# Kernel tuning notes

Hardware: AMD Instinct MI355X
Metric: run time of the kernel (lower is better)

The kernel has to match this reference:

```python
import jax, jax.numpy as jnp
import numpy as np

T, D, R, C, L = 4096, 512, 32, 32, 2  # time, input, trace, context, num_blocks
NEG_SLOPE = 0.01
EPS = 1e-5  # eqx LayerNorm default


def _layernorm(x, g, b):
    m = jnp.mean(x, -1, keepdims=True)
    v = jnp.var(x, -1, keepdims=True)
    return g * (x - m) * jax.lax.rsqrt(v + EPS) + b


def _ffa_scan(a, b, pre, s0, start):
    # a:[R], b:[C], pre:[T,R,C] real>=0, s0:[1,R,C] complex64, start:[T] bool
    ab = jax.lax.complex(jnp.broadcast_to(-jnp.abs(a)[:, None], (R, C)),
                         jnp.broadcast_to(b[None, :], (R, C)))  # log decay+rotation
    ts = jnp.concatenate([jnp.zeros((1,), jnp.float32), jnp.ones((T,), jnp.float32)])
    vals = jnp.concatenate([s0, pre.astype(jnp.complex64)], axis=0)  # [T+1,R,C]
    rst = jnp.concatenate([jnp.zeros((1,), bool), start])

    def op(l, r):
        tl, sl, dl = l
        tr, sr, dr = r
        decay = jnp.exp(ab[None, :, :] * tr[:, None, None])  # gamma^{t_r}
        s = jnp.where(dr[:, None, None], sr, sr + sl * decay)
        t = jnp.where(dr, tr, tl + tr)
        return (t, s, dl | dr)

    _, states, _ = jax.lax.associative_scan(op, (ts, vals, rst))
    return states[1:]  # [T,R,C]


def _forward(x, start_b, state_real, state_imag, Wt, Wc, a, b,
             W0, b0, g0, beta0, W1, b1, g1, beta1):
    h = x
    z = x
    for i in range(L):
        tr = h @ Wt[i].T  # [T,R]
        ct = h @ Wc[i].T  # [T,R] (source maps context proj to trace_size too; R==C)
        pre = jnp.abs(tr[:, :, None] * ct[:, None, :])  # [T,R,C] outer product
        pre = pre / (1e-8 + jnp.sum(pre, axis=(-2, -1), keepdims=True))
        s0 = jax.lax.complex(state_real[i], state_imag[i])  # [1,R,C]
        states = _ffa_scan(a[i], b[i], pre, s0, start_b)
        s = states.reshape(T, R * C)
        mag = jnp.log1p(jnp.abs(s))
        ang = jnp.angle(s)
        scaled = jnp.concatenate([mag * jnp.sin(ang), mag * jnp.cos(ang)], axis=-1)  # [T,2RC]
        z = jax.nn.leaky_relu(_layernorm(scaled @ W0[i].T + b0[i], g0[i], beta0[i]), NEG_SLOPE)
        z = jax.nn.leaky_relu(_layernorm(z @ W1[i].T + b1[i], g1[i], beta1[i]), NEG_SLOPE)
        h = h + z  # residual feeds next block; NSFFM returns last block's z
    return z


def setup_inputs() -> dict:
    key = jax.random.key(0)
    ks = jax.random.split(key, 8)
    x = jax.random.normal(ks[0], (T, D), jnp.float32)
    start = jax.random.randint(ks[1], (T,), 0, 2).astype(jnp.int32)
    next_done = jax.random.randint(ks[2], (T,), 0, 2).astype(jnp.int32)
    Wt = jax.random.normal(ks[3], (L, R, D), jnp.float32) / np.sqrt(D)
    Wc = jax.random.normal(ks[4], (L, R, D), jnp.float32) / np.sqrt(D)
    # ffa.init: a = linspace decays, b = log-spaced angular frequencies
    a = jnp.broadcast_to(jnp.linspace(1e-6, 0.5, R, dtype=jnp.float32)[None], (L, R)).copy()
    b = jnp.broadcast_to((2 * jnp.pi / jnp.exp(jnp.linspace(np.log(1.0), np.log(1024.0), C))).astype(jnp.float32)[None], (L, C)).copy()
    W0 = jax.random.normal(ks[5], (L, D, 2 * R * C), jnp.float32) * 0.01  # default_init scale=0.01
    W1 = jax.random.normal(ks[6], (L, D, D), jnp.float32) / np.sqrt(D)
    return {
        'x': x, 'start': start, 'next_done': next_done,
        'state_real': jnp.zeros((L, 1, R, C), jnp.float32),
        'state_imag': jnp.zeros((L, 1, R, C), jnp.float32),
        'Wt': Wt, 'Wc': Wc, 'a': a, 'b': b,
        'W0': W0, 'b0': jnp.zeros((L, D), jnp.float32),
        'g0': jnp.ones((L, D), jnp.float32), 'beta0': jnp.zeros((L, D), jnp.float32),
        'W1': W1, 'b1': jnp.zeros((L, D), jnp.float32),
        'g1': jnp.ones((L, D), jnp.float32), 'beta1': jnp.zeros((L, D), jnp.float32),
    }


def reference(x, start, next_done, state_real, state_imag, Wt, Wc, a, b,
              W0, b0, g0, beta0, W1, b1, g1, beta1):
    del next_done  # not used in the scan math (kept for interface parity)
    start_b = start.astype(bool)
    return _forward(x, start_b, state_real, state_imag, Wt, Wc, a, b,
                    W0, b0, g0, beta0, W1, b1, g1, beta1)
```

## Files before the change

kernel.cpp:

```cpp
#include <hip/hip_runtime.h>
#include <math.h>

#define TT 4096
#define DD 512
#define RR 32
#define CC 32
#define RC 1024
#define LL 2
#define CHUNK 32
#define NCHUNK 128
#define NEG_SLOPE 0.01f
#define LN_EPS 1e-5f

typedef __attribute__((ext_vector_type(8))) __bf16 bf16x8;
typedef __attribute__((ext_vector_type(4))) float f32x4;

__device__ __forceinline__ unsigned short f2bf(float f) {
    unsigned int u = __builtin_bit_cast(unsigned int, f);
    u += 0x7fffu + ((u >> 16) & 1u);
    return (unsigned short)(u >> 16);
}

#define NX4  524288
#define NW04 524288
#define NW14 131072
#define NCV  (NX4 + NW04 + NW14)
#define NPK  16384
__global__ __launch_bounds__(256) void setup_kernel(const float4* __restrict__ x,
                                                    const float4* __restrict__ W0,
                                                    const float4* __restrict__ W1,
                                                    const float* __restrict__ Wt,
                                                    const float* __restrict__ Wc,
                                                    ushort4* __restrict__ xb,
                                                    ushort4* __restrict__ W0b,
                                                    ushort4* __restrict__ W1b,
                                                    ushort4* __restrict__ Wtc) {
    int i = blockIdx.x * 256 + threadIdx.x;
    float4 v;
    ushort4* dst;
    int j;
    if (i < NCV) {
        const float4* src;
        if (i < NX4) { src = x; dst = xb; j = i; }
        else if (i < NX4 + NW04) { src = W0; dst = W0b; j = i - NX4; }
        else { src = W1; dst = W1b; j = i - NX4 - NW04; }
        v = src[j];
    } else {
        int ii = i - NCV;
        if (ii >= NPK) return;
        int e = ii * 4;
        int l = e >> 15;
        int r = (e >> 9) & 63;
        int k = e & 511;
        v = (r < 32) ? *(const float4*)&Wt[((size_t)l * 32 + r) * 512 + k]
                     : *(const float4*)&Wc[((size_t)l * 32 + (r - 32)) * 512 + k];
        dst = Wtc; j = ii;
    }
    ushort4 o;
    o.x = f2bf(v.x); o.y = f2bf(v.y); o.z = f2bf(v.z); o.w = f2bf(v.w);
    dst[j] = o;
}

__global__ __launch_bounds__(256) void proj_denom_kernel(const unsigned short* __restrict__ A,
                                                         const unsigned short* __restrict__ B,
                                                         float* __restrict__ tcabs) {
    __shared__ __align__(16) unsigned short As[64 * 32];
    __shared__ __align__(16) unsigned short Bs[64 * 32];
    const int tid = threadIdx.x;
    const int w = tid >> 6, lane = tid & 63;
    const int bm = blockIdx.x * 64;
    const int K = 512;
    const int srow = tid >> 2;
    const int sl = tid & 3;
    const int sswz = (sl ^ ((srow >> 1) & 3)) * 8;
    const unsigned short* gA = A + (size_t)(bm + srow) * K + sl * 8;
    const unsigned short* gB = B + (size_t)srow * K + sl * 8;
    const int wA = srow * 32 + sswz;
    const int wB = srow * 32 + sswz;
    const int fr = lane & 15, hi = lane >> 4;
    const int kslot = hi ^ ((fr >> 1) & 3);
    f32x4 acc0 = {}, acc1 = {}, acc2 = {}, acc3 = {};

    uint4 va = *(const uint4*)gA;
    uint4 vb = *(const uint4*)gB;
    for (int k0 = 0; k0 < K; k0 += 32) {
        __syncthreads();
        *(uint4*)&As[wA] = va;
        *(uint4*)&Bs[wB] = vb;
        __syncthreads();
        if (k0 + 32 < K) {
            va = *(const uint4*)(gA + k0 + 32);
            vb = *(const uint4*)(gB + k0 + 32);
        }
        const int arow = w * 16 + fr;
        bf16x8 af = *(const bf16x8*)&As[arow * 32 + kslot * 8];
        bf16x8 b0 = *(const bf16x8*)&Bs[(0 * 16 + fr) * 32 + kslot * 8];
        bf16x8 b1 = *(const bf16x8*)&Bs[(1 * 16 + fr) * 32 + kslot * 8];
        bf16x8 b2 = *(const bf16x8*)&Bs[(2 * 16 + fr) * 32 + kslot * 8];
        bf16x8 b3 = *(const bf16x8*)&Bs[(3 * 16 + fr) * 32 + kslot * 8];
        acc0 = __builtin_amdgcn_mfma_f32_16x16x32_bf16(af, b0, acc0, 0, 0, 0);
        acc1 = __builtin_amdgcn_mfma_f32_16x16x32_bf16(af, b1, acc1, 0, 0, 0);
        acc2 = __builtin_amdgcn_mfma_f32_16x16x32_bf16(af, b2, acc2, 0, 0, 0);
        acc3 = __builtin_amdgcn_mfma_f32_16x16x32_bf16(af, b3, acc3, 0, 0, 0);
    }
#pragma unroll
    for (int q = 0; q < 4; ++q) {
        float a0 = fabsf(acc0[q]), a1 = fabsf(acc1[q]);
        float a2 = fabsf(acc2[q]), a3 = fabsf(acc3[q]);
        float st = a0 + a1, sc = a2 + a3;
        st += __shfl_xor(st, 1); sc += __shfl_xor(sc, 1);
        st += __shfl_xor(st, 2); sc += __shfl_xor(sc, 2);
        st += __shfl_xor(st, 4); sc += __shfl_xor(sc, 4);
        st += __shfl_xor(st, 8); sc += __shfl_xor(sc, 8);
        float inv = 1.f / (1e-8f + st * sc);
        size_t rb = (size_t)(bm + w * 16 + hi * 4 + q) * 64;
        tcabs[rb + fr]      = a0 * inv;
        tcabs[rb + fr + 16] = a1 * inv;
        tcabs[rb + fr + 32] = a2;
        tcabs[rb + fr + 48] = a3;
    }
}

__global__ __launch_bounds__(256) void scan_pass1(const float* __restrict__ tcabs,
                                                  const int* __restrict__ start,
                                                  const float* __restrict__ a,
                                                  const float* __restrict__ b,
                                                  float4* __restrict__ ab4) {
    int tid = blockIdx.x * 256 + threadIdx.x;
    int rc = tid & (RC - 1);
    int chunk = tid >> 10;
    int r = rc >> 5, c = rc & 31;
    float e = expf(-fabsf(a[r]));
    float gr = e * cosf(b[c]);
    float gi = e * sinf(b[c]);
    float alr = 1.f, ali = 0.f, ber = 0.f, bei = 0.f;
    int t0 = chunk * CHUNK;
    for (int j = 0; j < CHUNK; ++j) {
        int t = t0 + j;
        float pre = tcabs[t * 64 + r] * tcabs[t * 64 + 32 + c];
        if (start[t]) {
            alr = 0.f; ali = 0.f; ber = pre; bei = 0.f;
        } else {
            float nbr = pre + gr * ber - gi * bei;
            float nbi =       gr * bei + gi * ber;
            float nar = gr * alr - gi * ali;
            float nai = gr * ali + gi * alr;
            ber = nbr; bei = nbi; alr = nar; ali = nai;
        }
    }
    ab4[chunk * RC + rc] = make_float4(alr, ali, ber, bei);
}

__global__ __launch_bounds__(256) void scan_pass2f(const float* __restrict__ tcabs,
                                                   const float4* __restrict__ ab4,
                                                   const int* __restrict__ start,
                                                   const float* __restrict__ a,
                                                   const float* __restrict__ b,
                                                   const float* __restrict__ s0r,
                                                   const float* __restrict__ s0i,
                                                   unsigned short* __restrict__ scaled) {
    int bx = blockIdx.x;
    int chunk = bx >> 2;
    int rc = (bx & 3) * 256 + threadIdx.x;
    int r = rc >> 5, c = rc & 31;
    float e = expf(-fabsf(a[r]));
    float gr = e * cosf(b[c]);
    float gi = e * sinf(b[c]);
    float sr = s0r[rc], si = s0i[rc];
    int j = 0;
    for (; j + 8 <= chunk; j += 8) {
        float4 buf[8];
#pragma unroll
        for (int u = 0; u < 8; ++u) buf[u] = ab4[(j + u) * RC + rc];
#pragma unroll
        for (int u = 0; u < 8; ++u) {
            float nsr = buf[u].z + buf[u].x * sr - buf[u].y * si;
            float nsi = buf[u].w + buf[u].x * si + buf[u].y * sr;
            sr = nsr; si = nsi;
        }
    }
    for (; j < chunk; ++j) {
        float4 ab = ab4[j * RC + rc];
        float nsr = ab.z + ab.x * sr - ab.y * si;
        float nsi = ab.w + ab.x * si + ab.y * sr;
        sr = nsr; si = nsi;
    }
    int t0 = chunk * CHUNK;
    for (int jj = 0; jj < CHUNK; ++jj) {
        int t = t0 + jj;
        float pre = tcabs[t * 64 + r] * tcabs[t * 64 + 32 + c];
        if (start[t]) {
            sr = pre; si = 0.f;
        } else {
            float nsr = pre + gr * sr - gi * si;
            float nsi =       gr * si + gi * sr;
            sr = nsr; si = nsi;
        }
        float m = sqrtf(sr * sr + si * si);
        float mag = log1pf(m);
        float f = (m > 0.f) ? (mag / m) : 0.f;
        scaled[(size_t)t * 2048 + rc]        = f2bf(si * f);
        scaled[(size_t)t * 2048 + 1024 + rc] = f2bf(sr * f);
    }
}

template <int K, int N, int SPLITK>
__global__ __launch_bounds__(256) void gemm_bt_mfma(const unsigned short* __restrict__ A,
                                                    const unsigned short* __restrict__ B,
                                                    float* __restrict__ Cm) {
    __shared__ __align__(16) unsigned short As[128 * 64];
    __shared__ __align__(16) unsigned short Bs[64 * 64];
    const int tid = threadIdx.x;
    const int w = tid >> 6, lane = tid & 63;
    const int nwg = gridDim.x * gridDim.y * gridDim.z;
    const int id = blockIdx.x + gridDim.x * (blockIdx.y + gridDim.y * blockIdx.z);
    const int lid = (id & 7) * (nwg >> 3) + (id >> 3);
    const int bxs = lid % gridDim.x;
    const int t2 = lid / gridDim.x;
    const int bys = t2 % gridDim.y;
    const int bzs = t2 / gridDim.y;
    const int bm = bys * 128, bn = bxs * 64;
    const int kbeg = bzs * (K / SPLITK);
    const int kend = kbeg + (K / SPLITK);
    const int wr = w >> 1, wc = w & 1;
    const int srow = tid >> 3;
    const int k8 = tid & 7;
    const int swz = (k8 ^ (srow & 7)) * 8;
    const unsigned short* gA = A + (size_t)(bm + srow) * K + k8 * 8;
    const unsigned short* gB = B + (size_t)(bn + srow) * K + k8 * 8;
    const int wAb = srow * 64 + swz;
    const int fr = lane & 15, hi = lane >> 4;
    f32x4 acc[4][2] = {};

    uint4 va0 = *(const uint4*)(gA + kbeg);
    uint4 va1 = *(const uint4*)(gA + (size_t)32 * K + kbeg);
    uint4 va2 = *(const uint4*)(gA + (size_t)64 * K + kbeg);
    uint4 va3 = *(const uint4*)(gA + (size_t)96 * K + kbeg);
    uint4 vb0 = *(const uint4*)(gB + kbeg);
    uint4 vb1 = *(const uint4*)(gB + (size_t)32 * K + kbeg);
    for (int k0 = kbeg; k0 < kend; k0 += 64) {
        __syncthreads();
        *(uint4*)&As[wAb]        = va0;
        *(uint4*)&As[wAb + 2048] = va1;
        *(uint4*)&As[wAb + 4096] = va2;
        *(uint4*)&As[wAb + 6144] = va3;
        *(uint4*)&Bs[wAb]        = vb0;
        *(uint4*)&Bs[wAb + 2048] = vb1;
        __syncthreads();
        if (k0 + 64 < kend) {
            va0 = *(const uint4*)(gA + k0 + 64);
            va1 = *(const uint4*)(gA + (size_t)32 * K + k0 + 64);
            va2 = *(const uint4*)(gA + (size_t)64 * K + k0 + 64);
            va3 = *(const uint4*)(gA + (size_t)96 * K + k0 + 64);
            vb0 = *(const uint4*)(gB + k0 + 64);
            vb1 = *(const uint4*)(gB + (size_t)32 * K + k0 + 64);
        }
#pragma unroll
        for (int kk = 0; kk < 2; ++kk) {
            const int ks = kk * 4 + hi;
            bf16x8 af[4], bfv[2];
#pragma unroll
            for (int mi = 0; mi < 4; ++mi) {
                int row = wr * 64 + mi * 16 + fr;
                af[mi] = *(const bf16x8*)&As[row * 64 + ((ks ^ (row & 7)) * 8)];
            }
#pragma unroll
            for (int ni = 0; ni < 2; ++ni) {
                int row = wc * 32 + ni * 16 + fr;
                bfv[ni] = *(const bf16x8*)&Bs[row * 64 + ((ks ^ (row & 7)) * 8)];
            }
#pragma unroll
            for (int mi = 0; mi < 4; ++mi)
#pragma unroll
                for (int ni = 0; ni < 2; ++ni)
                    acc[mi][ni] = __builtin_amdgcn_mfma_f32_16x16x32_bf16(
                        af[mi], bfv[ni], acc[mi][ni], 0, 0, 0);
        }
    }
    float* Cz = Cm + (size_t)bzs * TT * N;
    const int ccol0 = bn + wc * 32 + fr;
    const int crow0 = bm + wr * 64 + hi * 4;
#pragma unroll
    for (int ni = 0; ni < 2; ++ni) {
        int col = ccol0 + ni * 16;
#pragma unroll
        for (int mi = 0; mi < 4; ++mi)
#pragma unroll
            for (int q = 0; q < 4; ++q)
                Cz[(size_t)(crow0 + mi * 16 + q) * N + col] = acc[mi][ni][q];
    }
}

__global__ __launch_bounds__(256) void ln_lrelu_kernel(const float* __restrict__ y0,
                                                       const float* __restrict__ y1,
                                                       const float* __restrict__ badd,
                                                       const float* __restrict__ g,
                                                       const float* __restrict__ be,
                                                       unsigned short* __restrict__ zb,
                                                       const float* __restrict__ res,
                                                       unsigned short* __restrict__ hbf,
                                                       float* __restrict__ fout) {
    const int lane = threadIdx.x & 63;
    const int row = blockIdx.x * 4 + (threadIdx.x >> 6);
    const size_t base = (size_t)row * 512 + lane * 8;
    const int cb = lane * 8;
    float4 p0a = *(const float4*)&y0[base];
    float4 p0b = *(const float4*)&y0[base + 4];
    float4 p1a = *(const float4*)&y1[base];
    float4 p1b = *(const float4*)&y1[base + 4];
    float4 ba = *(const float4*)&badd[cb];
    float4 bb = *(const float4*)&badd[cb + 4];
    float v[8];
    v[0] = p0a.x + p1a.x + ba.x; v[1] = p0a.y + p1a.y + ba.y;
    v[2] = p0a.z + p1a.z + ba.z; v[3] = p0a.w + p1a.w + ba.w;
    v[4] = p0b.x + p1b.x + bb.x; v[5] = p0b.y + p1b.y + bb.y;
    v[6] = p0b.z + p1b.z + bb.z; v[7] = p0b.w + p1b.w + bb.w;
    float s = 0.f, ss = 0.f;
#pragma unroll
    for (int j = 0; j < 8; ++j) { s += v[j]; ss += v[j] * v[j]; }
#pragma unroll
    for (int o = 1; o < 64; o <<= 1) {
        s  += __shfl_xor(s, o);
        ss += __shfl_xor(ss, o);
    }
    float m = s * (1.f / 512.f);
    float rs = rsqrtf(ss * (1.f / 512.f) - m * m + LN_EPS);
    float4 ga = *(const float4*)&g[cb];
    float4 gb = *(const float4*)&g[cb + 4];
    float4 ea = *(const float4*)&be[cb];
    float4 eb = *(const float4*)&be[cb + 4];
    float gg[8] = {ga.x, ga.y, ga.z, ga.w, gb.x, gb.y, gb.z, gb.w};
    float ee[8] = {ea.x, ea.y, ea.z, ea.w, eb.x, eb.y, eb.z, eb.w};
    float z[8];
#pragma unroll
    for (int j = 0; j < 8; ++j) {
        float zz = gg[j] * (v[j] - m) * rs + ee[j];
        z[j] = (zz > 0.f) ? zz : NEG_SLOPE * zz;
    }
    if (zb) {
        ushort4 o0, o1;
        o0.x = f2bf(z[0]); o0.y = f2bf(z[1]); o0.z = f2bf(z[2]); o0.w = f2bf(z[3]);
        o1.x = f2bf(z[4]); o1.y = f2bf(z[5]); o1.z = f2bf(z[6]); o1.w = f2bf(z[7]);
        *(ushort4*)&zb[base] = o0;
        *(ushort4*)&zb[base + 4] = o1;
    }
    if (hbf) {
        float4 ra = *(const float4*)&res[base];
        float4 rb2 = *(const float4*)&res[base + 4];
        ushort4 o0, o1;
        o0.x = f2bf(ra.x + z[0]); o0.y = f2bf(ra.y + z[1]);
        o0.z = f2bf(ra.z + z[2]); o0.w = f2bf(ra.w + z[3]);
        o1.x = f2bf(rb2.x + z[4]); o1.y = f2bf(rb2.y + z[5]);
        o1.z = f2bf(rb2.z + z[6]); o1.w = f2bf(rb2.w + z[7]);
        *(ushort4*)&hbf[base] = o0;
        *(ushort4*)&hbf[base + 4] = o1;
    }
    if (fout) {
        *(float4*)&fout[base] = make_float4(z[0], z[1], z[2], z[3]);
        *(float4*)&fout[base + 4] = make_float4(z[4], z[5], z[6], z[7]);
    }
}

extern "C" void kernel_launch(void* const* d_in, const int* in_sizes, int n_in,
                              void* d_out, int out_size, void* d_ws, size_t ws_size,
                              hipStream_t stream) {
    const float* x     = (const float*)d_in[0];
    const int*   start = (const int*)d_in[1];
    const float* s0r = (const float*)d_in[3];
    const float* s0i = (const float*)d_in[4];
    const float* Wt  = (const float*)d_in[5];
    const float* Wc  = (const float*)d_in[6];
    const float* a   = (const float*)d_in[7];
    const float* b   = (const float*)d_in[8];
    const float* W0  = (const float*)d_in[9];
    const float* b0  = (const float*)d_in[10];
    const float* g0  = (const float*)d_in[11];
    const float* be0 = (const float*)d_in[12];
    const float* W1  = (const float*)d_in[13];
    const float* b1  = (const float*)d_in[14];
    const float* g1  = (const float*)d_in[15];
    const float* be1 = (const float*)d_in[16];
    float* out = (float*)d_out;
    float* ws  = (float*)d_ws;

    float* p = ws;
    float* tcabs  = p; p += 262144;
    float4* ab4   = (float4*)p; p += 524288;
    unsigned short* scaled = (unsigned short*)p; p += 4194304;
    float* ybufp  = p; p += 4194304;
    unsigned short* zbuf_bf = (unsigned short*)p; p += 1048576;
    unsigned short* x_bf    = (unsigned short*)p; p += 1048576;
    unsigned short* h_bf    = (unsigned short*)p; p += 1048576;
    unsigned short* Wtcbf   = (unsigned short*)p; p += 32768;
    unsigned short* W0bf    = (unsigned short*)p; p += 1048576;
    unsigned short* W1bf    = (unsigned short*)p; p += 262144;

    setup_kernel<<<(NCV + NPK + 255) / 256, 256, 0, stream>>>(
        (const float4*)x, (const float4*)W0, (const float4*)W1, Wt, Wc,
        (ushort4*)x_bf, (ushort4*)W0bf, (ushort4*)W1bf, (ushort4*)Wtcbf);

    for (int i = 0; i < LL; ++i) {
        const unsigned short* hb = (i == 0) ? x_bf : h_bf;
        proj_denom_kernel<<<64, 256, 0, stream>>>(
            hb, Wtcbf + (size_t)i * 64 * 512, tcabs);
        scan_pass1<<<NCHUNK * RC / 256, 256, 0, stream>>>(
            tcabs, start, a + i * RR, b + i * CC, ab4);
        scan_pass2f<<<NCHUNK * 4, 256, 0, stream>>>(
            tcabs, ab4, start, a + i * RR, b + i * CC,
            s0r + i * RC, s0i + i * RC, scaled);
        gemm_bt_mfma<2048, 512, 2><<<dim3(8, 32, 2), 256, 0, stream>>>(
            scaled, W0bf + (size_t)i * 512 * 2048, ybufp);
        ln_lrelu_kernel<<<1024, 256, 0, stream>>>(
            ybufp, ybufp + (size_t)TT * 512, b0 + i * DD, g0 + i * DD, be0 + i * DD,
            zbuf_bf, nullptr, nullptr, nullptr);
        gemm_bt_mfma<512, 512, 2><<<dim3(8, 32, 2), 256, 0, stream>>>(
            zbuf_bf, W1bf + (size_t)i * 512 * 512, ybufp);
        ln_lrelu_kernel<<<1024, 256, 0, stream>>>(
            ybufp, ybufp + (size_t)TT * 512, b1 + i * DD, g1 + i * DD, be1 + i * DD,
            nullptr,
            (i < LL - 1) ? x : nullptr,
            (i < LL - 1) ? h_bf : nullptr,
            (i == LL - 1) ? out : nullptr);
    }
}
```

Baseline: 184.9 us.

## Store split-K GEMM partials in bf16, widen proj K-tile, balance scan chunks

The split-K GEMM partial outputs are now written as bf16 instead of fp32, which halves the traffic between the GEMMs and the layernorm kernels. The layernorm kernels convert these partials back to float before use. The projection kernel now stages a 64-wide K tile with an 8-way XOR swizzle and runs two MFMA steps per barrier, so it synchronises half as often. The scan pass-2 kernel interleaves short and long prefix chunks across blocks to balance load, and replaces sqrt plus divide with rsqrt. Rounding the partials to bf16 before summing them adds precision error.

```diff
diff --git a/kernel.cpp b/kernel.cpp
--- a/kernel.cpp
+++ b/kernel.cpp
@@ -19,6 +19,10 @@
     unsigned int u = __builtin_bit_cast(unsigned int, f);
     u += 0x7fffu + ((u >> 16) & 1u);
     return (unsigned short)(u >> 16);
+}
+__device__ __forceinline__ float bf2f(unsigned short s) {
+    unsigned int u = (unsigned int)s << 16;
+    return __builtin_bit_cast(float, u);
 }
 
 #define NX4  524288
@@ -64,44 +68,52 @@
 __global__ __launch_bounds__(256) void proj_denom_kernel(const unsigned short* __restrict__ A,
                                                          const unsigned short* __restrict__ B,
                                                          float* __restrict__ tcabs) {
-    __shared__ __align__(16) unsigned short As[64 * 32];
-    __shared__ __align__(16) unsigned short Bs[64 * 32];
+    __shared__ __align__(16) unsigned short As[64 * 64];
+    __shared__ __align__(16) unsigned short Bs[64 * 64];
     const int tid = threadIdx.x;
     const int w = tid >> 6, lane = tid & 63;
     const int bm = blockIdx.x * 64;
     const int K = 512;
-    const int srow = tid >> 2;
-    const int sl = tid & 3;
-    const int sswz = (sl ^ ((srow >> 1) & 3)) * 8;
-    const unsigned short* gA = A + (size_t)(bm + srow) * K + sl * 8;
-    const unsigned short* gB = B + (size_t)srow * K + sl * 8;
-    const int wA = srow * 32 + sswz;
-    const int wB = srow * 32 + sswz;
+    const int srow = tid >> 3;
+    const int k8 = tid & 7;
+    const int swz = (k8 ^ (srow & 7)) * 8;
+    const unsigned short* gA = A + (size_t)(bm + srow) * K + k8 * 8;
+    const unsigned short* gB = B + (size_t)srow * K + k8 * 8;
+    const int wb = srow * 64 + swz;
     const int fr = lane & 15, hi = lane >> 4;
-    const int kslot = hi ^ ((fr >> 1) & 3);
     f32x4 acc0 = {}, acc1 = {}, acc2 = {}, acc3 = {};
 
-    uint4 va = *(const uint4*)gA;
-    uint4 vb = *(const uint4*)gB;
-    for (int k0 = 0; k0 < K; k0 += 32) {
+    uint4 va0 = *(const uint4*)gA;
+    uint4 va1 = *(const uint4*)(gA + (size_t)32 * K);
+    uint4 vb0 = *(const uint4*)gB;
+    uint4 vb1 = *(const uint4*)(gB + (size_t)32 * K);
+    for (int k0 = 0; k0 < K; k0 += 64) {
         __syncthreads();
-        *(uint4*)&As[wA] = va;
-        *(uint4*)&Bs[wB] = vb;
+        *(uint4*)&As[wb]        = va0;
+        *(uint4*)&As[wb + 2048] = va1;
+        *(uint4*)&Bs[wb]        = vb0;
+        *(uint4*)&Bs[wb + 2048] = vb1;
         __syncthreads();
-        if (k0 + 32 < K) {
-            va = *(const uint4*)(gA + k0 + 32);
-            vb = *(const uint4*)(gB + k0 + 32);
+        if (k0 + 64 < K) {
+            va0 = *(const uint4*)(gA + k0 + 64);
+            va1 = *(const uint4*)(gA + (size_t)32 * K + k0 + 64);
+            vb0 = *(const uint4*)(gB + k0 + 64);
+            vb1 = *(const uint4*)(gB + (size_t)32 * K + k0 + 64);
         }
         const int arow = w * 16 + fr;
-        bf16x8 af = *(const bf16x8*)&As[arow * 32 + kslot * 8];
-        bf16x8 b0 = *(const bf16x8*)&Bs[(0 * 16 + fr) * 32 + kslot * 8];
-        bf16x8 b1 = *(const bf16x8*)&Bs[(1 * 16 + fr) * 32 + kslot * 8];
-        bf16x8 b2 = *(const bf16x8*)&Bs[(2 * 16 + fr) * 32 + kslot * 8];
-        bf16x8 b3 = *(const bf16x8*)&Bs[(3 * 16 + fr) * 32 + kslot * 8];
-        acc0 = __builtin_amdgcn_mfma_f32_16x16x32_bf16(af, b0, acc0, 0, 0, 0);
-        acc1 = __builtin_amdgcn_mfma_f32_16x16x32_bf16(af, b1, acc1, 0, 0, 0);
-        acc2 = __builtin_amdgcn_mfma_f32_16x16x32_bf16(af, b2, acc2, 0, 0, 0);
-        acc3 = __builtin_amdgcn_mfma_f32_16x16x32_bf16(af, b3, acc3, 0, 0, 0);
+#pragma unroll
+        for (int kk = 0; kk < 2; ++kk) {
+            const int ks = kk * 4 + hi;
+            bf16x8 af = *(const bf16x8*)&As[arow * 64 + ((ks ^ (arow & 7)) * 8)];
+            bf16x8 b0 = *(const bf16x8*)&Bs[(0 * 16 + fr) * 64 + ((ks ^ (fr & 7)) * 8)];
+            bf16x8 b1 = *(const bf16x8*)&Bs[(1 * 16 + fr) * 64 + ((ks ^ (fr & 7)) * 8)];
+            bf16x8 b2 = *(const bf16x8*)&Bs[(2 * 16 + fr) * 64 + ((ks ^ (fr & 7)) * 8)];
+            bf16x8 b3 = *(const bf16x8*)&Bs[(3 * 16 + fr) * 64 + ((ks ^ (fr & 7)) * 8)];
+            acc0 = __builtin_amdgcn_mfma_f32_16x16x32_bf16(af, b0, acc0, 0, 0, 0);
+            acc1 = __builtin_amdgcn_mfma_f32_16x16x32_bf16(af, b1, acc1, 0, 0, 0);
+            acc2 = __builtin_amdgcn_mfma_f32_16x16x32_bf16(af, b2, acc2, 0, 0, 0);
+            acc3 = __builtin_amdgcn_mfma_f32_16x16x32_bf16(af, b3, acc3, 0, 0, 0);
+        }
     }
 #pragma unroll
     for (int q = 0; q < 4; ++q) {
@@ -160,7 +172,8 @@
                                                    const float* __restrict__ s0i,
                                                    unsigned short* __restrict__ scaled) {
     int bx = blockIdx.x;
-    int chunk = bx >> 2;
+    int cid = bx >> 2;
+    int chunk = (cid & 1) ? (NCHUNK - 1 - (cid >> 1)) : (cid >> 1);
     int rc = (bx & 3) * 256 + threadIdx.x;
     int r = rc >> 5, c = rc & 31;
     float e = expf(-fabsf(a[r]));
@@ -196,9 +209,10 @@
             float nsi =       gr * si + gi * sr;
             sr = nsr; si = nsi;
         }
-        float m = sqrtf(sr * sr + si * si);
-        float mag = log1pf(m);
-        float f = (m > 0.f) ? (mag / m) : 0.f;
+        float m2 = sr * sr + si * si;
+        float rsq = rsqrtf(m2);
+        float m = m2 * rsq;
+        float f = (m2 > 0.f) ? log1pf(m) * rsq : 0.f;
         scaled[(size_t)t * 2048 + rc]        = f2bf(si * f);
         scaled[(size_t)t * 2048 + 1024 + rc] = f2bf(sr * f);
     }
@@ -207,7 +221,7 @@
 template <int K, int N, int SPLITK>
 __global__ __launch_bounds__(256) void gemm_bt_mfma(const unsigned short* __restrict__ A,
                                                     const unsigned short* __restrict__ B,
-                                                    float* __restrict__ Cm) {
+                                                    unsigned short* __restrict__ Cm) {
     __shared__ __align__(16) unsigned short As[128 * 64];
     __shared__ __align__(16) unsigned short Bs[64 * 64];
     const int tid = threadIdx.x;
@@ -277,7 +291,7 @@
                         af[mi], bfv[ni], acc[mi][ni], 0, 0, 0);
         }
     }
-    float* Cz = Cm + (size_t)bzs * TT * N;
+    unsigned short* Cz = Cm + (size_t)bzs * TT * N;
     const int ccol0 = bn + wc * 32 + fr;
     const int crow0 = bm + wr * 64 + hi * 4;
 #pragma unroll
@@ -287,12 +301,12 @@
         for (int mi = 0; mi < 4; ++mi)
 #pragma unroll
             for (int q = 0; q < 4; ++q)
-                Cz[(size_t)(crow0 + mi * 16 + q) * N + col] = acc[mi][ni][q];
-    }
-}
-
-__global__ __launch_bounds__(256) void ln_lrelu_kernel(const float* __restrict__ y0,
-                                                       const float* __restrict__ y1,
+                Cz[(size_t)(crow0 + mi * 16 + q) * N + col] = f2bf(acc[mi][ni][q]);
+    }
+}
+
+__global__ __launch_bounds__(256) void ln_lrelu_kernel(const unsigned short* __restrict__ y0,
+                                                       const unsigned short* __restrict__ y1,
                                                        const float* __restrict__ badd,
                                                        const float* __restrict__ g,
                                                        const float* __restrict__ be,
@@ -304,17 +318,21 @@
     const int row = blockIdx.x * 4 + (threadIdx.x >> 6);
     const size_t base = (size_t)row * 512 + lane * 8;
     const int cb = lane * 8;
-    float4 p0a = *(const float4*)&y0[base];
-    float4 p0b = *(const float4*)&y0[base + 4];
-    float4 p1a = *(const float4*)&y1[base];
-    float4 p1b = *(const float4*)&y1[base + 4];
+    ushort4 ua0 = *(const ushort4*)&y0[base];
+    ushort4 ua1 = *(const ushort4*)&y0[base + 4];
+    ushort4 ub0 = *(const ushort4*)&y1[base];
+    ushort4 ub1 = *(const ushort4*)&y1[base + 4];
     float4 ba = *(const float4*)&badd[cb];
     float4 bb = *(const float4*)&badd[cb + 4];
     float v[8];
-    v[0] = p0a.x + p1a.x + ba.x; v[1] = p0a.y + p1a.y + ba.y;
-    v[2] = p0a.z + p1a.z + ba.z; v[3] = p0a.w + p1a.w + ba.w;
-    v[4] = p0b.x + p1b.x + bb.x; v[5] = p0b.y + p1b.y + bb.y;
-    v[6] = p0b.z + p1b.z + bb.z; v[7] = p0b.w + p1b.w + bb.w;
+    v[0] = bf2f(ua0.x) + bf2f(ub0.x) + ba.x;
+    v[1] = bf2f(ua0.y) + bf2f(ub0.y) + ba.y;
+    v[2] = bf2f(ua0.z) + bf2f(ub0.z) + ba.z;
+    v[3] = bf2f(ua0.w) + bf2f(ub0.w) + ba.w;
+    v[4] = bf2f(ua1.x) + bf2f(ub1.x) + bb.x;
+    v[5] = bf2f(ua1.y) + bf2f(ub1.y) + bb.y;
+    v[6] = bf2f(ua1.z) + bf2f(ub1.z) + bb.z;
+    v[7] = bf2f(ua1.w) + bf2f(ub1.w) + bb.w;
     float s = 0.f, ss = 0.f;
 #pragma unroll
     for (int j = 0; j < 8; ++j) { s += v[j]; ss += v[j] * v[j]; }
@@ -387,7 +405,7 @@
     float* tcabs  = p; p += 262144;
     float4* ab4   = (float4*)p; p += 524288;
     unsigned short* scaled = (unsigned short*)p; p += 4194304;
-    float* ybufp  = p; p += 4194304;
+    unsigned short* ybufp_bf = (unsigned short*)p; p += 2097152;
     unsigned short* zbuf_bf = (unsigned short*)p; p += 1048576;
     unsigned short* x_bf    = (unsigned short*)p; p += 1048576;
     unsigned short* h_bf    = (unsigned short*)p; p += 1048576;
@@ -409,14 +427,14 @@
             tcabs, ab4, start, a + i * RR, b + i * CC,
             s0r + i * RC, s0i + i * RC, scaled);
         gemm_bt_mfma<2048, 512, 2><<<dim3(8, 32, 2), 256, 0, stream>>>(
-            scaled, W0bf + (size_t)i * 512 * 2048, ybufp);
+            scaled, W0bf + (size_t)i * 512 * 2048, ybufp_bf);
         ln_lrelu_kernel<<<1024, 256, 0, stream>>>(
-            ybufp, ybufp + (size_t)TT * 512, b0 + i * DD, g0 + i * DD, be0 + i * DD,
+            ybufp_bf, ybufp_bf + (size_t)TT * 512, b0 + i * DD, g0 + i * DD, be0 + i * DD,
             zbuf_bf, nullptr, nullptr, nullptr);
         gemm_bt_mfma<512, 512, 2><<<dim3(8, 32, 2), 256, 0, stream>>>(
-            zbuf_bf, W1bf + (size_t)i * 512 * 512, ybufp);
+            zbuf_bf, W1bf + (size_t)i * 512 * 512, ybufp_bf);
         ln_lrelu_kernel<<<1024, 256, 0, stream>>>(
-            ybufp, ybufp + (size_t)TT * 512, b1 + i * DD, g1 + i * DD, be1 + i * DD,
+            ybufp_bf, ybufp_bf + (size_t)TT * 512, b1 + i * DD, g1 + i * DD, be1 + i * DD,
             nullptr,
             (i < LL - 1) ? x : nullptr,
             (i < LL - 1) ? h_bf : nullptr,
```

New measurement: 178.5 us. -3.5%, faster.
